# Kernel tuning notes

Hardware: AMD Instinct MI355X
Metric: run time of the kernel (lower is better)

Reference implementation:

```python
import jax, jax.numpy as jnp
import numpy as np

N = 8192
D_IN = 512
D_HID = 256
D_OUT = 128
NEG_SLOPE = 0.25
MASK_VAL = -1.0e12
EDGE_PROB = 0.004  # avg degree ~33


def _leaky(x):
    return jax.nn.leaky_relu(x, NEG_SLOPE)


def setup_inputs() -> dict:
    key = jax.random.key(0)
    ks = jax.random.split(key, 9)
    x = jax.random.normal(ks[0], (N, D_IN), jnp.float32)
    # sparse-ish normalized adjacency, stored dense (torch uses sparse mm / to_dense)
    vals = jax.random.uniform(ks[1], (N, N), jnp.float32)
    mask = jax.random.uniform(ks[2], (N, N)) < EDGE_PROB
    adj = jnp.where(mask, vals, 0.0).astype(jnp.float32)
    W1 = jax.random.normal(ks[3], (D_IN, D_HID), jnp.float32) * (2.0 / (D_IN + D_HID)) ** 0.5
    b1 = jnp.zeros((D_HID,), jnp.float32)
    W2 = jax.random.normal(ks[4], (D_HID, D_HID), jnp.float32) * (1.0 / D_HID) ** 0.5
    b2 = jnp.zeros((D_HID,), jnp.float32)
    Wg = jax.random.normal(ks[5], (D_HID, D_OUT), jnp.float32) * (2.0 / (D_HID + D_OUT)) ** 0.5
    a = jax.random.normal(ks[6], (2 * D_OUT, 1), jnp.float32) * 0.1
    return dict(x=x, adj=adj, W1=W1, b1=b1, W2=W2, b2=b2, Wg=Wg, a=a)


def reference(x, adj, W1, b1, W2, b2, Wg, a):
    # GCN layer 1: adj @ (x @ W1) + b1, leaky_relu (dropout p=0 / eval -> identity)
    x1 = _leaky(adj @ (x @ W1) + b1)
    # GCN layer 2
    x2 = _leaky(adj @ (x1 @ W2) + b2)
    # GAT layer: h = x2 @ Wg; e[i,j] = leaky_relu([h_i || h_j] @ a)
    # identical to leaky_relu((h@a1)_i + (h@a2)_j) without the O(N^2*2F) concat
    h = x2 @ Wg                              # [N, D_OUT]
    a1 = a[:D_OUT, 0]
    a2 = a[D_OUT:, 0]
    e = _leaky((h @ a1)[:, None] + (h @ a2)[None, :])  # [N, N]
    att = jnp.where(adj > 0, e, MASK_VAL)
    att = jax.nn.softmax(att, axis=1)
    h_prime = att @ h                        # [N, D_OUT] (concat=False -> no elu)
    out = _leaky(h_prime)
    mu = out[:, : D_OUT // 2]
    logvar = out[:, D_OUT // 2 :]
    return mu, logvar
```

## Files before the change

### kernel.cpp

```cpp
#include <hip/hip_runtime.h>

typedef unsigned short u16;
typedef u16 u16x4 __attribute__((ext_vector_type(4)));
typedef __bf16 bf16x8 __attribute__((ext_vector_type(8)));
typedef float f32x4 __attribute__((ext_vector_type(4)));

#define NROW 8192
#define CAP 128
#define D_IN 512
#define D_HID 256
#define D_OUT 128

__device__ __forceinline__ float leaky_f(float x) { return x > 0.f ? x : 0.25f * x; }

__device__ __forceinline__ u16 f2bf_rne(float f) {
  unsigned u = __float_as_uint(f);
  u += 0x7fffu + ((u >> 16) & 1u);
  return (u16)(u >> 16);
}
__device__ __forceinline__ float bf2f(u16 v) { return __uint_as_float(((unsigned)v) << 16); }
__device__ __forceinline__ void split_bf16(float f, u16& hi, u16& lo) {
  hi = f2bf_rne(f);
  float fh = __uint_as_float(((unsigned)hi) << 16);
  lo = f2bf_rne(f - fh);
}

__global__ __launch_bounds__(256) void k_packw(
    const float* __restrict__ W1, u16* __restrict__ B1,
    const float* __restrict__ W2, u16* __restrict__ B2,
    const float* __restrict__ Wg, u16* __restrict__ B3) {
  const float* W; u16* Bt; int K, Nc, idx;
  int pb = blockIdx.x;
  if (pb < 64)      { W = W1; Bt = B1; K = D_IN;  Nc = D_HID; idx = pb * 256 + threadIdx.x; }
  else if (pb < 96) { W = W2; Bt = B2; K = D_HID; Nc = D_HID; idx = (pb - 64) * 256 + threadIdx.x; }
  else              { W = Wg; Bt = B3; K = D_HID; Nc = D_OUT; idx = (pb - 96) * 256 + threadIdx.x; }
  int ko8 = K >> 3;
  int n = idx / ko8, k0 = (idx % ko8) << 3;
  alignas(16) u16 hh[8], ll[8];
#pragma unroll
  for (int j = 0; j < 8; ++j) {
    float f = W[(size_t)(k0 + j) * Nc + n];
    split_bf16(f, hh[j], ll[j]);
  }
  size_t ro = (size_t)n * 2 * K;
  *(uint4*)(Bt + ro + k0)     = *(const uint4*)hh;
  *(uint4*)(Bt + ro + K + k0) = *(const uint4*)ll;
}

__global__ __launch_bounds__(256) void k_csr_gemm1(const float* __restrict__ adj,
    int* __restrict__ cnt, int* __restrict__ cols, float* __restrict__ vals,
    const float* __restrict__ X, const u16* __restrict__ Bt, u16* __restrict__ C) {
  __shared__ alignas(16) u16 Ah[64 * 40], Al[64 * 40];
  __shared__ alignas(16) u16 Bh[64 * 40], Bl[64 * 40];
  __shared__ int csrc;
  int b = blockIdx.x;
  int tid = threadIdx.x;
  if (b < 512) {
    const int N = D_HID, K = D_IN;
    int bm = (b >> 2) * 64, bn = (b & 3) * 64;
    int wave = tid >> 6, lane = tid & 63, l15 = lane & 15, quad = lane >> 4;
    f32x4 acc[4] = {};
    int ar = tid >> 2, aj = (tid & 3) << 3;
    const float* Xrow = X + (size_t)(bm + ar) * K + aj;
    const u16* Brow = Bt + (size_t)(bn + ar) * (2 * K) + aj;
    for (int k0 = 0; k0 < K; k0 += 32) {
      alignas(16) u16 hh[8], ll[8];
      float xv[8];
      *(float4*)(xv)     = *(const float4*)(Xrow + k0);
      *(float4*)(xv + 4) = *(const float4*)(Xrow + k0 + 4);
#pragma unroll
      for (int e = 0; e < 8; ++e) split_bf16(xv[e], hh[e], ll[e]);
      *(uint4*)(&Ah[ar * 40 + aj]) = *(const uint4*)hh;
      *(uint4*)(&Al[ar * 40 + aj]) = *(const uint4*)ll;
      *(uint4*)(&Bh[ar * 40 + aj]) = *(const uint4*)(Brow + k0);
      *(uint4*)(&Bl[ar * 40 + aj]) = *(const uint4*)(Brow + K + k0);
      __syncthreads();
      bf16x8 afh = *(const bf16x8*)(&Ah[(wave * 16 + l15) * 40 + quad * 8]);
      bf16x8 afl = *(const bf16x8*)(&Al[(wave * 16 + l15) * 40 + quad * 8]);
#pragma unroll
      for (int c = 0; c < 4; ++c) {
        bf16x8 bfh = *(const bf16x8*)(&Bh[(c * 16 + l15) * 40 + quad * 8]);
        bf16x8 bfl = *(const bf16x8*)(&Bl[(c * 16 + l15) * 40 + quad * 8]);
        acc[c] = __builtin_amdgcn_mfma_f32_16x16x32_bf16(afh, bfh, acc[c], 0, 0, 0);
        acc[c] = __builtin_amdgcn_mfma_f32_16x16x32_bf16(afh, bfl, acc[c], 0, 0, 0);
        acc[c] = __builtin_amdgcn_mfma_f32_16x16x32_bf16(afl, bfh, acc[c], 0, 0, 0);
      }
      __syncthreads();
    }
#pragma unroll
    for (int c = 0; c < 4; ++c)
#pragma unroll
      for (int rg = 0; rg < 4; ++rg) {
        int rowi = bm + wave * 16 + quad * 4 + rg;
        int coli = bn + c * 16 + l15;
        C[(size_t)rowi * N + coli] = f2bf_rne(acc[c][rg]);
      }
    return;
  }
  int i = b - 512;
  if (tid == 0) csrc = 0;
  __syncthreads();
  int lane = tid & 63;
  const float4* row = (const float4*)(adj + (size_t)i * NROW);
  for (int j4 = tid; j4 < NROW / 4; j4 += 256) {
    float4 v = row[j4];
    int base = j4 * 4;
    bool p0 = v.x > 0.f, p1 = v.y > 0.f, p2 = v.z > 0.f, p3 = v.w > 0.f;
    unsigned long long m0 = __ballot(p0), m1 = __ballot(p1);
    unsigned long long m2 = __ballot(p2), m3 = __ballot(p3);
    int c0 = __popcll(m0), c1 = __popcll(m1), c2 = __popcll(m2), c3 = __popcll(m3);
    int tot = c0 + c1 + c2 + c3;
    if (tot) {
      int wbase = 0;
      if (lane == 0) wbase = atomicAdd(&csrc, tot);
      wbase = __shfl(wbase, 0);
      unsigned long long lm = (1ULL << lane) - 1ULL;
      int o0 = wbase + __popcll(m0 & lm);
      int o1 = wbase + c0 + __popcll(m1 & lm);
      int o2 = wbase + c0 + c1 + __popcll(m2 & lm);
      int o3 = wbase + c0 + c1 + c2 + __popcll(m3 & lm);
      if (p0 && o0 < CAP) { cols[i*CAP+o0] = base;   vals[i*CAP+o0] = v.x; }
      if (p1 && o1 < CAP) { cols[i*CAP+o1] = base+1; vals[i*CAP+o1] = v.y; }
      if (p2 && o2 < CAP) { cols[i*CAP+o2] = base+2; vals[i*CAP+o2] = v.z; }
      if (p3 && o3 < CAP) { cols[i*CAP+o3] = base+3; vals[i*CAP+o3] = v.w; }
    }
  }
  __syncthreads();
  if (tid == 0) cnt[i] = (csrc < CAP) ? csrc : CAP;
}


__device__ __forceinline__ float4 gather_row256(const u16* __restrict__ Hin,
    const int* scw, const float* svw, int n, int lane) {
  float4 acc = {0.f, 0.f, 0.f, 0.f};
  int k = 0;
  for (; k + 7 < n; k += 8) {
    int   c0 = scw[k],     c1 = scw[k + 1], c2 = scw[k + 2], c3 = scw[k + 3];
    int   c4 = scw[k + 4], c5 = scw[k + 5], c6 = scw[k + 6], c7 = scw[k + 7];
    float w0 = svw[k],     w1 = svw[k + 1], w2 = svw[k + 2], w3 = svw[k + 3];
    float w4 = svw[k + 4], w5 = svw[k + 5], w6 = svw[k + 6], w7 = svw[k + 7];
    u16x4 v0 = *(const u16x4*)(Hin + (size_t)c0 * 256 + 4 * lane);
    u16x4 v1 = *(const u16x4*)(Hin + (size_t)c1 * 256 + 4 * lane);
    u16x4 v2 = *(const u16x4*)(Hin + (size_t)c2 * 256 + 4 * lane);
    u16x4 v3 = *(const u16x4*)(Hin + (size_t)c3 * 256 + 4 * lane);
    u16x4 v4 = *(const u16x4*)(Hin + (size_t)c4 * 256 + 4 * lane);
    u16x4 v5 = *(const u16x4*)(Hin + (size_t)c5 * 256 + 4 * lane);
    u16x4 v6 = *(const u16x4*)(Hin + (size_t)c6 * 256 + 4 * lane);
    u16x4 v7 = *(const u16x4*)(Hin + (size_t)c7 * 256 + 4 * lane);
    acc.x = fmaf(w0, bf2f(v0[0]), acc.x); acc.y = fmaf(w0, bf2f(v0[1]), acc.y);
    acc.z = fmaf(w0, bf2f(v0[2]), acc.z); acc.w = fmaf(w0, bf2f(v0[3]), acc.w);
    acc.x = fmaf(w1, bf2f(v1[0]), acc.x); acc.y = fmaf(w1, bf2f(v1[1]), acc.y);
    acc.z = fmaf(w1, bf2f(v1[2]), acc.z); acc.w = fmaf(w1, bf2f(v1[3]), acc.w);
    acc.x = fmaf(w2, bf2f(v2[0]), acc.x); acc.y = fmaf(w2, bf2f(v2[1]), acc.y);
    acc.z = fmaf(w2, bf2f(v2[2]), acc.z); acc.w = fmaf(w2, bf2f(v2[3]), acc.w);
    acc.x = fmaf(w3, bf2f(v3[0]), acc.x); acc.y = fmaf(w3, bf2f(v3[1]), acc.y);
    acc.z = fmaf(w3, bf2f(v3[2]), acc.z); acc.w = fmaf(w3, bf2f(v3[3]), acc.w);
    acc.x = fmaf(w4, bf2f(v4[0]), acc.x); acc.y = fmaf(w4, bf2f(v4[1]), acc.y);
    acc.z = fmaf(w4, bf2f(v4[2]), acc.z); acc.w = fmaf(w4, bf2f(v4[3]), acc.w);
    acc.x = fmaf(w5, bf2f(v5[0]), acc.x); acc.y = fmaf(w5, bf2f(v5[1]), acc.y);
    acc.z = fmaf(w5, bf2f(v5[2]), acc.z); acc.w = fmaf(w5, bf2f(v5[3]), acc.w);
    acc.x = fmaf(w6, bf2f(v6[0]), acc.x); acc.y = fmaf(w6, bf2f(v6[1]), acc.y);
    acc.z = fmaf(w6, bf2f(v6[2]), acc.z); acc.w = fmaf(w6, bf2f(v6[3]), acc.w);
    acc.x = fmaf(w7, bf2f(v7[0]), acc.x); acc.y = fmaf(w7, bf2f(v7[1]), acc.y);
    acc.z = fmaf(w7, bf2f(v7[2]), acc.z); acc.w = fmaf(w7, bf2f(v7[3]), acc.w);
  }
  for (; k < n; ++k) {
    float wv = svw[k];
    u16x4 v = *(const u16x4*)(Hin + (size_t)scw[k] * 256 + 4 * lane);
    acc.x = fmaf(wv, bf2f(v[0]), acc.x); acc.y = fmaf(wv, bf2f(v[1]), acc.y);
    acc.z = fmaf(wv, bf2f(v[2]), acc.z); acc.w = fmaf(wv, bf2f(v[3]), acc.w);
  }
  return acc;
}

__device__ __forceinline__ void spmm_row_to_lds(const u16* __restrict__ Hin,
    const int* scw, const float* svw, int n, int lane, float4 bv,
    u16* AhF, u16* AlF, int r) {
  float4 acc = gather_row256(Hin, scw, svw, n, lane);
  float r4[4] = { leaky_f(acc.x + bv.x), leaky_f(acc.y + bv.y),
                  leaky_f(acc.z + bv.z), leaky_f(acc.w + bv.w) };
  u16x4 hi4, lo4;
#pragma unroll
  for (int e = 0; e < 4; ++e) { u16 hh, ll; split_bf16(r4[e], hh, ll); hi4[e] = hh; lo4[e] = ll; }
  int dst = (lane >> 3) * 640 + r * 40 + (lane & 7) * 4;
  *(u16x4*)(&AhF[dst]) = hi4;
  *(u16x4*)(&AlF[dst]) = lo4;
}

__global__ __launch_bounds__(512) void k_fuse1(const u16* __restrict__ Hin,
    const float* __restrict__ bias, const int* __restrict__ cnt,
    const int* __restrict__ cols, const float* __restrict__ vals,
    const u16* __restrict__ Bt, u16* __restrict__ Cout) {
  __shared__ alignas(16) u16 AhF[8 * 16 * 40], AlF[8 * 16 * 40];
  __shared__ int   sc[16 * CAP];
  __shared__ float sv[16 * CAP];
  int tid = threadIdx.x;
  int wave = tid >> 6, lane = tid & 63, l15 = lane & 15, quad = lane >> 4;
  int bm = blockIdx.x * 16;
  int r0 = wave * 2, r1 = r0 + 1;
  int i0 = bm + r0, i1 = bm + r1;
  int n0 = cnt[i0], n1 = cnt[i1];
  int* sc0 = sc + r0 * CAP;  float* sv0 = sv + r0 * CAP;
  int* sc1 = sc + r1 * CAP;  float* sv1 = sv + r1 * CAP;
  if (lane < n0)      { sc0[lane]      = cols[i0*CAP+lane];    sv0[lane]      = vals[i0*CAP+lane]; }
  if (lane + 64 < n0) { sc0[lane + 64] = cols[i0*CAP+lane+64]; sv0[lane + 64] = vals[i0*CAP+lane+64]; }
  if (lane < n1)      { sc1[lane]      = cols[i1*CAP+lane];    sv1[lane]      = vals[i1*CAP+lane]; }
  if (lane + 64 < n1) { sc1[lane + 64] = cols[i1*CAP+lane+64]; sv1[lane + 64] = vals[i1*CAP+lane+64]; }
  float4 bv = ((const float4*)bias)[lane];
  spmm_row_to_lds(Hin, sc0, sv0, n0, lane, bv, AhF, AlF, r0);
  spmm_row_to_lds(Hin, sc1, sv1, n1, lane, bv, AhF, AlF, r1);
  __syncthreads();
  f32x4 acc[2] = {};
#pragma unroll
  for (int k0 = 0; k0 < D_HID; k0 += 32) {
    bf16x8 afh = *(const bf16x8*)(&AhF[(k0 >> 5) * 640 + l15 * 40 + quad * 8]);
    bf16x8 afl = *(const bf16x8*)(&AlF[(k0 >> 5) * 640 + l15 * 40 + quad * 8]);
#pragma unroll
    for (int c = 0; c < 2; ++c) {
      int col = wave * 32 + c * 16 + l15;
      const u16* bp = Bt + (size_t)col * (2 * D_HID) + k0 + quad * 8;
      bf16x8 bfh = *(const bf16x8*)(bp);
      bf16x8 bfl = *(const bf16x8*)(bp + D_HID);
      acc[c] = __builtin_amdgcn_mfma_f32_16x16x32_bf16(afh, bfh, acc[c], 0, 0, 0);
      acc[c] = __builtin_amdgcn_mfma_f32_16x16x32_bf16(afh, bfl, acc[c], 0, 0, 0);
      acc[c] = __builtin_amdgcn_mfma_f32_16x16x32_bf16(afl, bfh, acc[c], 0, 0, 0);
    }
  }
#pragma unroll
  for (int c = 0; c < 2; ++c)
#pragma unroll
    for (int rg = 0; rg < 4; ++rg) {
      int rowi = bm + quad * 4 + rg;
      int coli = wave * 32 + c * 16 + l15;
      Cout[(size_t)rowi * 256 + coli] = f2bf_rne(acc[c][rg]);
    }
}

__global__ __launch_bounds__(512) void k_fuse2(const u16* __restrict__ Hin,
    const float* __restrict__ bias, const int* __restrict__ cnt,
    const int* __restrict__ cols, const float* __restrict__ vals,
    const u16* __restrict__ Bt, u16* __restrict__ Hb,
    const float* __restrict__ aptr, float* __restrict__ s1, float* __restrict__ s2) {
  __shared__ alignas(16) u16 AhF[8 * 16 * 40], AlF[8 * 16 * 40];
  __shared__ int   sc[16 * CAP];
  __shared__ float sv[16 * CAP];
  __shared__ float sp1[8][16], sp2[8][16];
  int tid = threadIdx.x;
  int wave = tid >> 6, lane = tid & 63, l15 = lane & 15, quad = lane >> 4;
  int bm = blockIdx.x * 16;
  int r0 = wave * 2, r1 = r0 + 1;
  int i0 = bm + r0, i1 = bm + r1;
  int n0 = cnt[i0], n1 = cnt[i1];
  int* sc0 = sc + r0 * CAP;  float* sv0 = sv + r0 * CAP;
  int* sc1 = sc + r1 * CAP;  float* sv1 = sv + r1 * CAP;
  if (lane < n0)      { sc0[lane]      = cols[i0*CAP+lane];    sv0[lane]      = vals[i0*CAP+lane]; }
  if (lane + 64 < n0) { sc0[lane + 64] = cols[i0*CAP+lane+64]; sv0[lane + 64] = vals[i0*CAP+lane+64]; }
  if (lane < n1)      { sc1[lane]      = cols[i1*CAP+lane];    sv1[lane]      = vals[i1*CAP+lane]; }
  if (lane + 64 < n1) { sc1[lane + 64] = cols[i1*CAP+lane+64]; sv1[lane + 64] = vals[i1*CAP+lane+64]; }
  float4 bv = ((const float4*)bias)[lane];
  spmm_row_to_lds(Hin, sc0, sv0, n0, lane, bv, AhF, AlF, r0);
  spmm_row_to_lds(Hin, sc1, sv1, n1, lane, bv, AhF, AlF, r1);
  __syncthreads();
  f32x4 acc = {};
#pragma unroll
  for (int k0 = 0; k0 < D_HID; k0 += 32) {
    bf16x8 afh = *(const bf16x8*)(&AhF[(k0 >> 5) * 640 + l15 * 40 + quad * 8]);
    bf16x8 afl = *(const bf16x8*)(&AlF[(k0 >> 5) * 640 + l15 * 40 + quad * 8]);
    int col = wave * 16 + l15;
    const u16* bp = Bt + (size_t)col * (2 * D_HID) + k0 + quad * 8;
    bf16x8 bfh = *(const bf16x8*)(bp);
    bf16x8 bfl = *(const bf16x8*)(bp + D_HID);
    acc = __builtin_amdgcn_mfma_f32_16x16x32_bf16(afh, bfh, acc, 0, 0, 0);
    acc = __builtin_amdgcn_mfma_f32_16x16x32_bf16(afh, bfl, acc, 0, 0, 0);
    acc = __builtin_amdgcn_mfma_f32_16x16x32_bf16(afl, bfh, acc, 0, 0, 0);
  }
#pragma unroll
  for (int rg = 0; rg < 4; ++rg) {
    int rowi = bm + quad * 4 + rg;
    int coli = wave * 16 + l15;
    Hb[(size_t)rowi * 128 + coli] = f2bf_rne(acc[rg]);
  }
  float a1v = aptr[wave * 16 + l15];
  float a2v = aptr[128 + wave * 16 + l15];
#pragma unroll
  for (int rg = 0; rg < 4; ++rg) {
    float p1 = acc[rg] * a1v;
    float p2 = acc[rg] * a2v;
#pragma unroll
    for (int m = 1; m < 16; m <<= 1) { p1 += __shfl_xor(p1, m); p2 += __shfl_xor(p2, m); }
    if (l15 == 0) {
      int rloc = quad * 4 + rg;
      sp1[wave][rloc] = p1; sp2[wave][rloc] = p2;
    }
  }
  __syncthreads();
  if (tid < 16) {
    float t1 = 0.f, t2 = 0.f;
#pragma unroll
    for (int wv = 0; wv < 8; ++wv) { t1 += sp1[wv][tid]; t2 += sp2[wv][tid]; }
    s1[bm + tid] = t1;
    s2[bm + tid] = t2;
  }
}

__global__ __launch_bounds__(256) void k_attn(const u16* __restrict__ Hb,
    const float* __restrict__ s1, const float* __restrict__ s2,
    const int* __restrict__ cnt, const int* __restrict__ cols, float* __restrict__ out) {
  __shared__ int sc[4][CAP];
  __shared__ float sp[4][CAP];
  int w = threadIdx.x >> 6, lane = threadIdx.x & 63;
  int i = blockIdx.x * 4 + w;
  int n = cnt[i];
  float s1i = s1[i];
  float e0 = -1e30f, e1 = -1e30f;
  if (lane < n)      { int c = cols[i * CAP + lane];      sc[w][lane]      = c; e0 = leaky_f(s1i + s2[c]); }
  if (lane + 64 < n) { int c = cols[i * CAP + lane + 64]; sc[w][lane + 64] = c; e1 = leaky_f(s1i + s2[c]); }
  float m = fmaxf(e0, e1);
#pragma unroll
  for (int o = 32; o > 0; o >>= 1) m = fmaxf(m, __shfl_xor(m, o));
  float p0 = (lane < n)      ? expf(e0 - m) : 0.f;
  float p1 = (lane + 64 < n) ? expf(e1 - m) : 0.f;
  if (lane < n)      sp[w][lane]      = p0;
  if (lane + 64 < n) sp[w][lane + 64] = p1;
  float s = p0 + p1;
#pragma unroll
  for (int o = 32; o > 0; o >>= 1) s += __shfl_xor(s, o);
  float inv = (n > 0) ? 1.0f / s : 0.f;
  __syncthreads();
  int half = lane >> 5, t32 = lane & 31;
  float4 acc = {0.f, 0.f, 0.f, 0.f};
  int k = half;
  for (; k + 6 < n; k += 8) {
    int   c0 = sc[w][k],     c1 = sc[w][k + 2], c2 = sc[w][k + 4], c3 = sc[w][k + 6];
    float w0 = sp[w][k],     w1 = sp[w][k + 2], w2 = sp[w][k + 4], w3 = sp[w][k + 6];
    u16x4 a0 = *(const u16x4*)(Hb + (size_t)c0 * 128 + 4 * t32);
    u16x4 a1 = *(const u16x4*)(Hb + (size_t)c1 * 128 + 4 * t32);
    u16x4 a2 = *(const u16x4*)(Hb + (size_t)c2 * 128 + 4 * t32);
    u16x4 a3 = *(const u16x4*)(Hb + (size_t)c3 * 128 + 4 * t32);
    acc.x = fmaf(w0, bf2f(a0[0]), acc.x); acc.y = fmaf(w0, bf2f(a0[1]), acc.y);
    acc.z = fmaf(w0, bf2f(a0[2]), acc.z); acc.w = fmaf(w0, bf2f(a0[3]), acc.w);
    acc.x = fmaf(w1, bf2f(a1[0]), acc.x); acc.y = fmaf(w1, bf2f(a1[1]), acc.y);
    acc.z = fmaf(w1, bf2f(a1[2]), acc.z); acc.w = fmaf(w1, bf2f(a1[3]), acc.w);
    acc.x = fmaf(w2, bf2f(a2[0]), acc.x); acc.y = fmaf(w2, bf2f(a2[1]), acc.y);
    acc.z = fmaf(w2, bf2f(a2[2]), acc.z); acc.w = fmaf(w2, bf2f(a2[3]), acc.w);
    acc.x = fmaf(w3, bf2f(a3[0]), acc.x); acc.y = fmaf(w3, bf2f(a3[1]), acc.y);
    acc.z = fmaf(w3, bf2f(a3[2]), acc.z); acc.w = fmaf(w3, bf2f(a3[3]), acc.w);
  }
  for (; k < n; k += 2) {
    float wv = sp[w][k];
    u16x4 a = *(const u16x4*)(Hb + (size_t)sc[w][k] * 128 + 4 * t32);
    acc.x = fmaf(wv, bf2f(a[0]), acc.x); acc.y = fmaf(wv, bf2f(a[1]), acc.y);
    acc.z = fmaf(wv, bf2f(a[2]), acc.z); acc.w = fmaf(wv, bf2f(a[3]), acc.w);
  }
  acc.x += __shfl_xor(acc.x, 32);
  acc.y += __shfl_xor(acc.y, 32);
  acc.z += __shfl_xor(acc.z, 32);
  acc.w += __shfl_xor(acc.w, 32);
  if (lane < 32) {
    float4 r;
    r.x = leaky_f(acc.x * inv);
    r.y = leaky_f(acc.y * inv);
    r.z = leaky_f(acc.z * inv);
    r.w = leaky_f(acc.w * inv);
    float4* o4 = (float4*)out;
    if (lane < 16) o4[(size_t)i * 16 + lane] = r;
    else           o4[(size_t)NROW * 16 + (size_t)i * 16 + (lane - 16)] = r;
  }
}

extern "C" void kernel_launch(void* const* d_in, const int* in_sizes, int n_in,
                              void* d_out, int out_size, void* d_ws, size_t ws_size,
                              hipStream_t stream) {
  const float* x   = (const float*)d_in[0];
  const float* adj = (const float*)d_in[1];
  const float* W1  = (const float*)d_in[2];
  const float* b1  = (const float*)d_in[3];
  const float* W2  = (const float*)d_in[4];
  const float* b2  = (const float*)d_in[5];
  const float* Wg  = (const float*)d_in[6];
  const float* a   = (const float*)d_in[7];
  float* out = (float*)d_out;

  char* ws = (char*)d_ws;
  int*   row_cnt  = (int*)  (ws + 0);
  int*   row_cols = (int*)  (ws + 32768);
  float* row_vals = (float*)(ws + 4227072);
  u16*   B1t      = (u16*)  (ws + 8421376);
  u16*   B2t      = (u16*)  (ws + 8945664);
  u16*   B3t      = (u16*)  (ws + 9207808);
  float* s1       = (float*)(ws + 9338880);
  float* s2       = (float*)(ws + 9371648);
  u16*   hbf      = (u16*)  (ws + 9404416);
  u16*   H0T2     = (u16*)  (ws + 13598720);
  u16*   T2       = (u16*)  (ws + 21987328);

  k_packw<<<112, 256, 0, stream>>>(W1, B1t, W2, B2t, Wg, B3t);
  k_csr_gemm1<<<512 + NROW, 256, 0, stream>>>(adj, row_cnt, row_cols, row_vals, x, B1t, H0T2);
  k_fuse1<<<NROW / 16, 512, 0, stream>>>(H0T2, b1, row_cnt, row_cols, row_vals, B2t, T2);
  k_fuse2<<<NROW / 16, 512, 0, stream>>>(T2, b2, row_cnt, row_cols, row_vals, B3t, hbf, a, s1, s2);
  k_attn<<<NROW / 4, 256, 0, stream>>>(hbf, s1, s2, row_cnt, row_cols, out);
}
```

Before: 438.3 us.

## Fold weight packing into CSR/GEMM1 kernel and batch gathers for more loads in flight

Removes the separate weight-packing launch. GEMM1 now reads W1 directly and splits it into bf16 hi/lo on the fly, while extra blocks appended to the CSR/GEMM1 grid pack W2 and Wg. The two-row SpMM in the fused kernels is interleaved so each iteration issues 16 independent gathers, and the attention gather loop is unrolled to 8 loads per step. Together these cut launch overhead and raise memory-level parallelism, at the cost of strided W1 reads repeated per GEMM tile and higher register pressure.

```diff
diff --git a/kernel.cpp b/kernel.cpp
--- a/kernel.cpp
+++ b/kernel.cpp
@@ -25,31 +25,11 @@
   lo = f2bf_rne(f - fh);
 }
 
-__global__ __launch_bounds__(256) void k_packw(
-    const float* __restrict__ W1, u16* __restrict__ B1,
+__global__ __launch_bounds__(256) void k_csr_gemm1(const float* __restrict__ adj,
+    int* __restrict__ cnt, int* __restrict__ cols, float* __restrict__ vals,
+    const float* __restrict__ X, const float* __restrict__ W1, u16* __restrict__ C,
     const float* __restrict__ W2, u16* __restrict__ B2,
     const float* __restrict__ Wg, u16* __restrict__ B3) {
-  const float* W; u16* Bt; int K, Nc, idx;
-  int pb = blockIdx.x;
-  if (pb < 64)      { W = W1; Bt = B1; K = D_IN;  Nc = D_HID; idx = pb * 256 + threadIdx.x; }
-  else if (pb < 96) { W = W2; Bt = B2; K = D_HID; Nc = D_HID; idx = (pb - 64) * 256 + threadIdx.x; }
-  else              { W = Wg; Bt = B3; K = D_HID; Nc = D_OUT; idx = (pb - 96) * 256 + threadIdx.x; }
-  int ko8 = K >> 3;
-  int n = idx / ko8, k0 = (idx % ko8) << 3;
-  alignas(16) u16 hh[8], ll[8];
-#pragma unroll
-  for (int j = 0; j < 8; ++j) {
-    float f = W[(size_t)(k0 + j) * Nc + n];
-    split_bf16(f, hh[j], ll[j]);
-  }
-  size_t ro = (size_t)n * 2 * K;
-  *(uint4*)(Bt + ro + k0)     = *(const uint4*)hh;
-  *(uint4*)(Bt + ro + K + k0) = *(const uint4*)ll;
-}
-
-__global__ __launch_bounds__(256) void k_csr_gemm1(const float* __restrict__ adj,
-    int* __restrict__ cnt, int* __restrict__ cols, float* __restrict__ vals,
-    const float* __restrict__ X, const u16* __restrict__ Bt, u16* __restrict__ C) {
   __shared__ alignas(16) u16 Ah[64 * 40], Al[64 * 40];
   __shared__ alignas(16) u16 Bh[64 * 40], Bl[64 * 40];
   __shared__ int csrc;
@@ -62,7 +42,7 @@
     f32x4 acc[4] = {};
     int ar = tid >> 2, aj = (tid & 3) << 3;
     const float* Xrow = X + (size_t)(bm + ar) * K + aj;
-    const u16* Brow = Bt + (size_t)(bn + ar) * (2 * K) + aj;
+    const float* Wcol = W1 + bn + ar;
     for (int k0 = 0; k0 < K; k0 += 32) {
       alignas(16) u16 hh[8], ll[8];
       float xv[8];
@@ -72,8 +52,13 @@
       for (int e = 0; e < 8; ++e) split_bf16(xv[e], hh[e], ll[e]);
       *(uint4*)(&Ah[ar * 40 + aj]) = *(const uint4*)hh;
       *(uint4*)(&Al[ar * 40 + aj]) = *(const uint4*)ll;
-      *(uint4*)(&Bh[ar * 40 + aj]) = *(const uint4*)(Brow + k0);
-      *(uint4*)(&Bl[ar * 40 + aj]) = *(const uint4*)(Brow + K + k0);
+      float wv[8];
+#pragma unroll
+      for (int j = 0; j < 8; ++j) wv[j] = Wcol[(size_t)(k0 + aj + j) * 256];
+#pragma unroll
+      for (int j = 0; j < 8; ++j) split_bf16(wv[j], hh[j], ll[j]);
+      *(uint4*)(&Bh[ar * 40 + aj]) = *(const uint4*)hh;
+      *(uint4*)(&Bl[ar * 40 + aj]) = *(const uint4*)ll;
       __syncthreads();
       bf16x8 afh = *(const bf16x8*)(&Ah[(wave * 16 + l15) * 40 + quad * 8]);
       bf16x8 afl = *(const bf16x8*)(&Al[(wave * 16 + l15) * 40 + quad * 8]);
@@ -95,6 +80,24 @@
         int coli = bn + c * 16 + l15;
         C[(size_t)rowi * N + coli] = f2bf_rne(acc[c][rg]);
       }
+    return;
+  }
+  if (b >= 512 + NROW) {
+    int pb = b - (512 + NROW);
+    const float* W; u16* Bt; int K, Nc, idx;
+    if (pb < 32) { W = W2; Bt = B2; K = D_HID; Nc = D_HID; idx = pb * 256 + tid; }
+    else         { W = Wg; Bt = B3; K = D_HID; Nc = D_OUT; idx = (pb - 32) * 256 + tid; }
+    int ko8 = K >> 3;
+    int n = idx / ko8, k0 = (idx % ko8) << 3;
+    alignas(16) u16 hh[8], ll[8];
+#pragma unroll
+    for (int j = 0; j < 8; ++j) {
+      float f = W[(size_t)(k0 + j) * Nc + n];
+      split_bf16(f, hh[j], ll[j]);
+    }
+    size_t ro = (size_t)n * 2 * K;
+    *(uint4*)(Bt + ro + k0)     = *(const uint4*)hh;
+    *(uint4*)(Bt + ro + K + k0) = *(const uint4*)ll;
     return;
   }
   int i = b - 512;
@@ -130,10 +133,8 @@
 }
 
 
-__device__ __forceinline__ float4 gather_row256(const u16* __restrict__ Hin,
-    const int* scw, const float* svw, int n, int lane) {
-  float4 acc = {0.f, 0.f, 0.f, 0.f};
-  int k = 0;
+__device__ __forceinline__ float4 gather_tail256(const u16* __restrict__ Hin,
+    const int* scw, const float* svw, int k, int n, int lane, float4 acc) {
   for (; k + 7 < n; k += 8) {
     int   c0 = scw[k],     c1 = scw[k + 1], c2 = scw[k + 2], c3 = scw[k + 3];
     int   c4 = scw[k + 4], c5 = scw[k + 5], c6 = scw[k + 6], c7 = scw[k + 7];
@@ -173,18 +174,47 @@
   return acc;
 }
 
-__device__ __forceinline__ void spmm_row_to_lds(const u16* __restrict__ Hin,
-    const int* scw, const float* svw, int n, int lane, float4 bv,
-    u16* AhF, u16* AlF, int r) {
-  float4 acc = gather_row256(Hin, scw, svw, n, lane);
-  float r4[4] = { leaky_f(acc.x + bv.x), leaky_f(acc.y + bv.y),
-                  leaky_f(acc.z + bv.z), leaky_f(acc.w + bv.w) };
+__device__ __forceinline__ void spmm_rows2_to_lds(const u16* __restrict__ Hin,
+    const int* sc0, const float* sv0, int n0,
+    const int* sc1, const float* sv1, int n1,
+    int lane, float4 bv, u16* AhF, u16* AlF, int r0, int r1) {
+  float4 a0 = {0.f, 0.f, 0.f, 0.f}, a1 = {0.f, 0.f, 0.f, 0.f};
+  int nmin = n0 < n1 ? n0 : n1;
+  int k = 0;
+  for (; k + 7 < nmin; k += 8) {
+    float wA[8], wB[8]; u16x4 vA[8], vB[8];
+#pragma unroll
+    for (int j = 0; j < 8; ++j) { wA[j] = sv0[k + j]; wB[j] = sv1[k + j]; }
+#pragma unroll
+    for (int j = 0; j < 8; ++j) {
+      vA[j] = *(const u16x4*)(Hin + (size_t)sc0[k + j] * 256 + 4 * lane);
+      vB[j] = *(const u16x4*)(Hin + (size_t)sc1[k + j] * 256 + 4 * lane);
+    }
+#pragma unroll
+    for (int j = 0; j < 8; ++j) {
+      a0.x = fmaf(wA[j], bf2f(vA[j][0]), a0.x); a0.y = fmaf(wA[j], bf2f(vA[j][1]), a0.y);
+      a0.z = fmaf(wA[j], bf2f(vA[j][2]), a0.z); a0.w = fmaf(wA[j], bf2f(vA[j][3]), a0.w);
+      a1.x = fmaf(wB[j], bf2f(vB[j][0]), a1.x); a1.y = fmaf(wB[j], bf2f(vB[j][1]), a1.y);
+      a1.z = fmaf(wB[j], bf2f(vB[j][2]), a1.z); a1.w = fmaf(wB[j], bf2f(vB[j][3]), a1.w);
+    }
+  }
+  a0 = gather_tail256(Hin, sc0, sv0, k, n0, lane, a0);
+  a1 = gather_tail256(Hin, sc1, sv1, k, n1, lane, a1);
+  float q0[4] = { leaky_f(a0.x + bv.x), leaky_f(a0.y + bv.y),
+                  leaky_f(a0.z + bv.z), leaky_f(a0.w + bv.w) };
+  float q1[4] = { leaky_f(a1.x + bv.x), leaky_f(a1.y + bv.y),
+                  leaky_f(a1.z + bv.z), leaky_f(a1.w + bv.w) };
   u16x4 hi4, lo4;
 #pragma unroll
-  for (int e = 0; e < 4; ++e) { u16 hh, ll; split_bf16(r4[e], hh, ll); hi4[e] = hh; lo4[e] = ll; }
-  int dst = (lane >> 3) * 640 + r * 40 + (lane & 7) * 4;
-  *(u16x4*)(&AhF[dst]) = hi4;
-  *(u16x4*)(&AlF[dst]) = lo4;
+  for (int e = 0; e < 4; ++e) { u16 hh, ll; split_bf16(q0[e], hh, ll); hi4[e] = hh; lo4[e] = ll; }
+  int dst0 = (lane >> 3) * 640 + r0 * 40 + (lane & 7) * 4;
+  *(u16x4*)(&AhF[dst0]) = hi4;
+  *(u16x4*)(&AlF[dst0]) = lo4;
+#pragma unroll
+  for (int e = 0; e < 4; ++e) { u16 hh, ll; split_bf16(q1[e], hh, ll); hi4[e] = hh; lo4[e] = ll; }
+  int dst1 = (lane >> 3) * 640 + r1 * 40 + (lane & 7) * 4;
+  *(u16x4*)(&AhF[dst1]) = hi4;
+  *(u16x4*)(&AlF[dst1]) = lo4;
 }
 
 __global__ __launch_bounds__(512) void k_fuse1(const u16* __restrict__ Hin,
@@ -207,8 +237,7 @@
   if (lane < n1)      { sc1[lane]      = cols[i1*CAP+lane];    sv1[lane]      = vals[i1*CAP+lane]; }
   if (lane + 64 < n1) { sc1[lane + 64] = cols[i1*CAP+lane+64]; sv1[lane + 64] = vals[i1*CAP+lane+64]; }
   float4 bv = ((const float4*)bias)[lane];
-  spmm_row_to_lds(Hin, sc0, sv0, n0, lane, bv, AhF, AlF, r0);
-  spmm_row_to_lds(Hin, sc1, sv1, n1, lane, bv, AhF, AlF, r1);
+  spmm_rows2_to_lds(Hin, sc0, sv0, n0, sc1, sv1, n1, lane, bv, AhF, AlF, r0, r1);
   __syncthreads();
   f32x4 acc[2] = {};
 #pragma unroll
@@ -258,8 +287,7 @@
   if (lane < n1)      { sc1[lane]      = cols[i1*CAP+lane];    sv1[lane]      = vals[i1*CAP+lane]; }
   if (lane + 64 < n1) { sc1[lane + 64] = cols[i1*CAP+lane+64]; sv1[lane + 64] = vals[i1*CAP+lane+64]; }
   float4 bv = ((const float4*)bias)[lane];
-  spmm_row_to_lds(Hin, sc0, sv0, n0, lane, bv, AhF, AlF, r0);
-  spmm_row_to_lds(Hin, sc1, sv1, n1, lane, bv, AhF, AlF, r1);
+  spmm_rows2_to_lds(Hin, sc0, sv0, n0, sc1, sv1, n1, lane, bv, AhF, AlF, r0, r1);
   __syncthreads();
   f32x4 acc = {};
 #pragma unroll
@@ -330,21 +358,17 @@
   int half = lane >> 5, t32 = lane & 31;
   float4 acc = {0.f, 0.f, 0.f, 0.f};
   int k = half;
-  for (; k + 6 < n; k += 8) {
-    int   c0 = sc[w][k],     c1 = sc[w][k + 2], c2 = sc[w][k + 4], c3 = sc[w][k + 6];
-    float w0 = sp[w][k],     w1 = sp[w][k + 2], w2 = sp[w][k + 4], w3 = sp[w][k + 6];
-    u16x4 a0 = *(const u16x4*)(Hb + (size_t)c0 * 128 + 4 * t32);
-    u16x4 a1 = *(const u16x4*)(Hb + (size_t)c1 * 128 + 4 * t32);
-    u16x4 a2 = *(const u16x4*)(Hb + (size_t)c2 * 128 + 4 * t32);
-    u16x4 a3 = *(const u16x4*)(Hb + (size_t)c3 * 128 + 4 * t32);
-    acc.x = fmaf(w0, bf2f(a0[0]), acc.x); acc.y = fmaf(w0, bf2f(a0[1]), acc.y);
-    acc.z = fmaf(w0, bf2f(a0[2]), acc.z); acc.w = fmaf(w0, bf2f(a0[3]), acc.w);
-    acc.x = fmaf(w1, bf2f(a1[0]), acc.x); acc.y = fmaf(w1, bf2f(a1[1]), acc.y);
-    acc.z = fmaf(w1, bf2f(a1[2]), acc.z); acc.w = fmaf(w1, bf2f(a1[3]), acc.w);
-    acc.x = fmaf(w2, bf2f(a2[0]), acc.x); acc.y = fmaf(w2, bf2f(a2[1]), acc.y);
-    acc.z = fmaf(w2, bf2f(a2[2]), acc.z); acc.w = fmaf(w2, bf2f(a2[3]), acc.w);
-    acc.x = fmaf(w3, bf2f(a3[0]), acc.x); acc.y = fmaf(w3, bf2f(a3[1]), acc.y);
-    acc.z = fmaf(w3, bf2f(a3[2]), acc.z); acc.w = fmaf(w3, bf2f(a3[3]), acc.w);
+  for (; k + 14 < n; k += 16) {
+    int cj[8]; float wj[8]; u16x4 aj[8];
+#pragma unroll
+    for (int j = 0; j < 8; ++j) { cj[j] = sc[w][k + 2*j]; wj[j] = sp[w][k + 2*j]; }
+#pragma unroll
+    for (int j = 0; j < 8; ++j) aj[j] = *(const u16x4*)(Hb + (size_t)cj[j] * 128 + 4 * t32);
+#pragma unroll
+    for (int j = 0; j < 8; ++j) {
+      acc.x = fmaf(wj[j], bf2f(aj[j][0]), acc.x); acc.y = fmaf(wj[j], bf2f(aj[j][1]), acc.y);
+      acc.z = fmaf(wj[j], bf2f(aj[j][2]), acc.z); acc.w = fmaf(wj[j], bf2f(aj[j][3]), acc.w);
+    }
   }
   for (; k < n; k += 2) {
     float wv = sp[w][k];
@@ -385,7 +409,6 @@
   int*   row_cnt  = (int*)  (ws + 0);
   int*   row_cols = (int*)  (ws + 32768);
   float* row_vals = (float*)(ws + 4227072);
-  u16*   B1t      = (u16*)  (ws + 8421376);
   u16*   B2t      = (u16*)  (ws + 8945664);
   u16*   B3t      = (u16*)  (ws + 9207808);
   float* s1       = (float*)(ws + 9338880);
@@ -394,8 +417,8 @@
   u16*   H0T2     = (u16*)  (ws + 13598720);
   u16*   T2       = (u16*)  (ws + 21987328);
 
-  k_packw<<<112, 256, 0, stream>>>(W1, B1t, W2, B2t, Wg, B3t);
-  k_csr_gemm1<<<512 + NROW, 256, 0, stream>>>(adj, row_cnt, row_cols, row_vals, x, B1t, H0T2);
+  k_csr_gemm1<<<512 + NROW + 48, 256, 0, stream>>>(adj, row_cnt, row_cols, row_vals,
+                                                   x, W1, H0T2, W2, B2t, Wg, B3t);
   k_fuse1<<<NROW / 16, 512, 0, stream>>>(H0T2, b1, row_cnt, row_cols, row_vals, B2t, T2);
   k_fuse2<<<NROW / 16, 512, 0, stream>>>(T2, b2, row_cnt, row_cols, row_vals, B3t, hbf, a, s1, s2);
   k_attn<<<NROW / 4, 256, 0, stream>>>(hbf, s1, s2, row_cnt, row_cols, out);
```

Result: no change. 442.5 us (+1.0%).
